# Optimization experiments

Measured on AMD Instinct MI355X. Metric: run time of the kernel, lower is better.

The kernel has to match this reference:

```python
import jax, jax.numpy as jnp
import numpy as np

N, E = 20000, 320000
IN_C, HID, OUT_C, HEADS = 512, 32, 40, 8
NEG_SLOPE = 0.2


def setup_inputs() -> dict:
    key = jax.random.key(0)
    ks = jax.random.split(key, 10)
    x = jax.random.normal(ks[0], (N, IN_C), dtype=jnp.float32)
    edge_index = jax.random.randint(ks[1], (2, E), 0, N, dtype=jnp.int64)
    s1 = 1.0 / np.sqrt(IN_C)
    s2 = 1.0 / np.sqrt(HEADS * HID)
    return {
        "x": x,
        "edge_index": edge_index,
        "w1": jax.random.normal(ks[2], (IN_C, HEADS * HID), dtype=jnp.float32) * s1,
        "att_src1": jax.random.normal(ks[3], (HEADS, HID), dtype=jnp.float32) * s2,
        "att_dst1": jax.random.normal(ks[4], (HEADS, HID), dtype=jnp.float32) * s2,
        "b1": jnp.zeros((HEADS * HID,), dtype=jnp.float32),
        "w2": jax.random.normal(ks[5], (HEADS * HID, OUT_C), dtype=jnp.float32) * s2,
        "att_src2": jax.random.normal(ks[6], (1, OUT_C), dtype=jnp.float32) * 0.15,
        "att_dst2": jax.random.normal(ks[7], (1, OUT_C), dtype=jnp.float32) * 0.15,
        "b2": jnp.zeros((OUT_C,), dtype=jnp.float32),
    }


def gat_conv(x, src, dst, w, att_src, att_dst, bias, heads, out_c, concat):
    n = x.shape[0]
    h = (x @ w).reshape(n, heads, out_c)            # [N,H,C]
    a_s = jnp.sum(h * att_src, axis=-1)             # [N,H]
    a_d = jnp.sum(h * att_dst, axis=-1)             # [N,H]
    e = jax.nn.leaky_relu(a_s[src] + a_d[dst], NEG_SLOPE)  # [E,H]
    # segment softmax over destination nodes (self-loops guarantee nonempty)
    m = jax.ops.segment_max(e, dst, num_segments=n)
    e = jnp.exp(e - m[dst])
    z = jax.ops.segment_sum(e, dst, num_segments=n)
    alpha = e / (z[dst] + 1e-16)                    # [E,H]
    msg = alpha[:, :, None] * h[src]                # [E,H,C]
    out = jax.ops.segment_sum(msg, dst, num_segments=n)  # [N,H,C]
    out = out.reshape(n, heads * out_c) if concat else out.mean(axis=1)
    return out + bias


def reference(x, edge_index, w1, att_src1, att_dst1, b1, w2, att_src2, att_dst2, b2):
    n = x.shape[0]
    loops = jnp.arange(n, dtype=edge_index.dtype)
    src = jnp.concatenate([edge_index[0], loops])
    dst = jnp.concatenate([edge_index[1], loops])
    h = gat_conv(x, src, dst, w1, att_src1, att_dst1, b1, HEADS, HID, True)
    h = jax.nn.elu(h)
    out = gat_conv(h, src, dst, w2, att_src2, att_dst2, b2, 1, OUT_C, False)
    return jax.nn.log_softmax(out, axis=1)
```

## Files before the change

### kernel.cpp

```cpp
#include <hip/hip_runtime.h>
#include <hip/hip_bf16.h>
#include <math.h>

#define N_NODES 20000
#define N_EDGES 320000
#define ET (N_EDGES + N_NODES)
#define IN_C 512
#define HEADS 8
#define HID 32
#define HH (HEADS * HID)
#define OUT_C 40
#define NEG_SLOPE 0.2f

typedef __attribute__((ext_vector_type(8))) short short8;
typedef __attribute__((ext_vector_type(4))) float floatx4;

static __device__ __forceinline__ unsigned short f2bf(float f) {
  __hip_bfloat16 h = __float2bfloat16(f);
  return *(unsigned short*)&h;
}
static __device__ __forceinline__ float bf2f_lo(unsigned int u) {
  return __uint_as_float(u << 16);
}
static __device__ __forceinline__ float bf2f_hi(unsigned int u) {
  return __uint_as_float(u & 0xFFFF0000u);
}

#define WCONV_BLOCKS (IN_C * HH / 256)
#define W2CONV_BLOCKS (HH * OUT_C / 256)
#define COUNT_BLOCKS ((ET + 255) / 256)
__global__ __launch_bounds__(256) void prep_kernel(
    const float* __restrict__ w1, const float* __restrict__ w2,
    const int* __restrict__ ei, unsigned short* __restrict__ wbT,
    unsigned short* __restrict__ w2bT, int* __restrict__ deg) {
  if (blockIdx.x < WCONV_BLOCKS) {
    int j = blockIdx.x * 256 + threadIdx.x;
    int k = j >> 8, n = j & 255;
    wbT[(size_t)n * IN_C + k] = f2bf(w1[j]);
  } else if (blockIdx.x < WCONV_BLOCKS + W2CONV_BLOCKS) {
    int j = (blockIdx.x - WCONV_BLOCKS) * 256 + threadIdx.x;
    int k = j / OUT_C, oc = j % OUT_C;
    w2bT[oc * HH + k] = f2bf(w2[j]);
  } else {
    int e = (blockIdx.x - WCONV_BLOCKS - W2CONV_BLOCKS) * 256 + threadIdx.x;
    if (e < ET) {
      int dst = (e < N_EDGES) ? ei[N_EDGES + e] : (e - N_EDGES);
      atomicAdd(&deg[dst], 1);
    }
  }
}

#define BM 64
#define BN 128
#define BK 32
#define APAD 40
#define GY ((N_NODES + BM - 1) / BM)
#define GEMM_BLOCKS (2 * GY)
__global__ __launch_bounds__(256) void gemm1_kernel(
    const float* __restrict__ X, const unsigned short* __restrict__ BT,
    const float* __restrict__ bias, unsigned short* __restrict__ C,
    const int* __restrict__ deg, int* __restrict__ offs, int* __restrict__ cursor) {
  if (blockIdx.x >= GEMM_BLOCKS) {
    __shared__ int wsum[4];
    int t = threadIdx.x;
    int4 buf[20];
    int s = 0;
    if (t < 250) {
      const int4* dp = (const int4*)deg + t * 20;
#pragma unroll
      for (int i = 0; i < 20; i++) {
        buf[i] = dp[i];
        s += buf[i].x + buf[i].y + buf[i].z + buf[i].w;
      }
    }
    int lane = t & 63, w = t >> 6;
    int inc = s;
    for (int o = 1; o < 64; o <<= 1) {
      int u = __shfl_up(inc, o, 64);
      if (lane >= o) inc += u;
    }
    if (lane == 63) wsum[w] = inc;
    __syncthreads();
    int waveOff = 0;
    for (int i = 0; i < w; i++) waveOff += wsum[i];
    int running = waveOff + inc - s;
    if (t < 250) {
      int base = t * 80;
#pragma unroll
      for (int i = 0; i < 20; i++) {
        int4 v = buf[i];
        int4 o;
        o.x = running;
        o.y = o.x + v.x;
        o.z = o.y + v.y;
        o.w = o.z + v.z;
        running = o.w + v.w;
        *(int4*)(offs + base + i * 4) = o;
        *(int4*)(cursor + base + i * 4) = o;
      }
    }
    if (t == 0) offs[N_NODES] = ET;
    return;
  }
  __shared__ unsigned short As[BM][APAD];
  __shared__ unsigned short Bs[BN][APAD];
  const int tid = threadIdx.x;
  const int lane = tid & 63, wave = tid >> 6;
  const int wm = (wave & 1) * 32;
  const int wn = (wave >> 1) * 64;
  const int r16 = lane & 15, q = lane >> 4;
  const int bx = blockIdx.x & 1, by = blockIdx.x >> 1;
  const int rowBase = by * BM;
  const int colBase = bx * BN;
  floatx4 acc[2][4] = {};

  for (int k0 = 0; k0 < IN_C; k0 += BK) {
    {
      int row = tid >> 2, kc = (tid & 3) * 8;
      int arow = rowBase + row;
      float4 v0 = make_float4(0.f, 0.f, 0.f, 0.f), v1 = v0;
      if (arow < N_NODES) {
        const float* p = X + (size_t)arow * IN_C + k0 + kc;
        v0 = *(const float4*)p;
        v1 = *(const float4*)(p + 4);
      }
      unsigned short tmp[8] = {f2bf(v0.x), f2bf(v0.y), f2bf(v0.z), f2bf(v0.w),
                               f2bf(v1.x), f2bf(v1.y), f2bf(v1.z), f2bf(v1.w)};
      *(float4*)&As[row][kc] = *(const float4*)tmp;
    }
#pragma unroll
    for (int i = 0; i < 2; i++) {
      int c = tid + i * 256;
      int row = c >> 2, kc = (c & 3) * 8;
      float4 v = *(const float4*)(BT + (size_t)(colBase + row) * IN_C + k0 + kc);
      *(float4*)&Bs[row][kc] = v;
    }
    __syncthreads();
    short8 afrag[2], bfrag[4];
#pragma unroll
    for (int mt = 0; mt < 2; mt++)
      afrag[mt] = *(const short8*)&As[wm + mt * 16 + r16][q * 8];
#pragma unroll
    for (int nt = 0; nt < 4; nt++)
      bfrag[nt] = *(const short8*)&Bs[wn + nt * 16 + r16][q * 8];
#pragma unroll
    for (int mt = 0; mt < 2; mt++)
#pragma unroll
      for (int nt = 0; nt < 4; nt++)
        acc[mt][nt] = __builtin_amdgcn_mfma_f32_16x16x32_bf16(
            afrag[mt], bfrag[nt], acc[mt][nt], 0, 0, 0);
    __syncthreads();
  }
#pragma unroll
  for (int mt = 0; mt < 2; mt++) {
#pragma unroll
    for (int nt = 0; nt < 4; nt++) {
      int col = colBase + wn + nt * 16 + r16;
      float bb = bias[col];
#pragma unroll
      for (int r = 0; r < 4; r++) {
        int row = rowBase + wm + mt * 16 + q * 4 + r;
        if (row < N_NODES) C[(size_t)row * HH + col] = f2bf(acc[mt][nt][r] + bb);
      }
    }
  }
}

#define FILL_BLOCKS ((ET + 255) / 256)
#define ATTN1_BLOCKS (N_NODES / 4)
__global__ __launch_bounds__(256) void fill_attn1_kernel(
    const int* __restrict__ ei, int* __restrict__ cursor, int* __restrict__ csr,
    const unsigned short* __restrict__ h1b, const float* __restrict__ asrc,
    const float* __restrict__ adst, float* __restrict__ as1, float* __restrict__ ad1) {
  if (blockIdx.x < FILL_BLOCKS) {
    int e = blockIdx.x * 256 + threadIdx.x;
    if (e >= ET) return;
    int src, dst;
    if (e < N_EDGES) { src = ei[e]; dst = ei[N_EDGES + e]; }
    else { src = e - N_EDGES; dst = src; }
    int pos = atomicAdd(&cursor[dst], 1);
    csr[pos] = src;
  } else {
    int wave = threadIdx.x >> 6, lane = threadIdx.x & 63;
    int n = (blockIdx.x - FILL_BLOCKS) * 4 + wave;
    int c4 = lane * 4;
    uint2 raw = *(const uint2*)(h1b + (size_t)n * HH + c4);
    float h0 = bf2f_lo(raw.x), h1 = bf2f_hi(raw.x);
    float h2 = bf2f_lo(raw.y), h3 = bf2f_hi(raw.y);
    float4 sa = *(const float4*)(asrc + c4);
    float4 sd = *(const float4*)(adst + c4);
    float ps = h0 * sa.x + h1 * sa.y + h2 * sa.z + h3 * sa.w;
    float pd = h0 * sd.x + h1 * sd.y + h2 * sd.z + h3 * sd.w;
#pragma unroll
    for (int o = 4; o > 0; o >>= 1) {
      ps += __shfl_down(ps, o, 8);
      pd += __shfl_down(pd, o, 8);
    }
    if ((lane & 7) == 0) {
      as1[n * HEADS + (lane >> 3)] = ps;
      ad1[n * HEADS + (lane >> 3)] = pd;
    }
  }
}

#define NPB 16
#define H2ROW 264
__global__ __launch_bounds__(256) void layer1_fused_kernel(
    const unsigned short* __restrict__ h1b, const float* __restrict__ as1,
    const float* __restrict__ ad1, const int* __restrict__ offs,
    const int* __restrict__ csr, const float* __restrict__ b1,
    const unsigned short* __restrict__ w2bT, const float* __restrict__ b2,
    const float* __restrict__ asrc2, const float* __restrict__ adst2,
    float* __restrict__ h3, float* __restrict__ as2, float* __restrict__ ad2) {
  __shared__ __align__(16) unsigned short h2s[NPB][H2ROW];
  __shared__ float psum[3][NPB], pdsum[3][NPB];
  const int tid = threadIdx.x;
  const int wave = tid >> 6, lane = tid & 63;
  const int r16 = lane & 15, q = lane >> 4;
  const int nodeBase = blockIdx.x * NPB;

  short8 bfrag[8];
  float sa = 0.f, sd = 0.f, b2c = 0.f;
  if (wave < 3) {
    int col = wave * 16 + r16;
    int colc = (col < OUT_C) ? col : 0;
#pragma unroll
    for (int s = 0; s < 8; s++)
      bfrag[s] = *(const short8*)(w2bT + colc * HH + s * 32 + q * 8);
    if (col < OUT_C) { sa = asrc2[col]; sd = adst2[col]; b2c = b2[col]; }
  }

  const int strm = lane >> 4;
  const int l16 = lane & 15;
  const int c16 = l16 * 16;
  const int head = l16 >> 1;
  float4 bb0 = *(const float4*)(b1 + c16);
  float4 bb1 = *(const float4*)(b1 + c16 + 4);
  float4 bb2 = *(const float4*)(b1 + c16 + 8);
  float4 bb3 = *(const float4*)(b1 + c16 + 12);
  for (int i = 0; i < 4; i++) {
    int local = wave * 4 + i;
    int n = nodeBase + local;
    int beg = offs[n], end = offs[n + 1];
    float ad = ad1[n * HEADS + head];
    float acc[16] = {};
    float l = 0.f;
#pragma unroll 2
    for (int k = beg + strm; k < end; k += 4) {
      int src = csr[k];
      float e = as1[src * HEADS + head] + ad;
      e = (e > 0.f) ? e : NEG_SLOPE * e;
      float p = __expf(e);
      l += p;
      const unsigned short* hp = h1b + ((unsigned)src << 8) + c16;
      uint4 r0 = *(const uint4*)hp;
      uint4 r1 = *(const uint4*)(hp + 8);
      acc[0]  = fmaf(p, bf2f_lo(r0.x), acc[0]);
      acc[1]  = fmaf(p, bf2f_hi(r0.x), acc[1]);
      acc[2]  = fmaf(p, bf2f_lo(r0.y), acc[2]);
      acc[3]  = fmaf(p, bf2f_hi(r0.y), acc[3]);
      acc[4]  = fmaf(p, bf2f_lo(r0.z), acc[4]);
      acc[5]  = fmaf(p, bf2f_hi(r0.z), acc[5]);
      acc[6]  = fmaf(p, bf2f_lo(r0.w), acc[6]);
      acc[7]  = fmaf(p, bf2f_hi(r0.w), acc[7]);
      acc[8]  = fmaf(p, bf2f_lo(r1.x), acc[8]);
      acc[9]  = fmaf(p, bf2f_hi(r1.x), acc[9]);
      acc[10] = fmaf(p, bf2f_lo(r1.y), acc[10]);
      acc[11] = fmaf(p, bf2f_hi(r1.y), acc[11]);
      acc[12] = fmaf(p, bf2f_lo(r1.z), acc[12]);
      acc[13] = fmaf(p, bf2f_hi(r1.z), acc[13]);
      acc[14] = fmaf(p, bf2f_lo(r1.w), acc[14]);
      acc[15] = fmaf(p, bf2f_hi(r1.w), acc[15]);
    }
#pragma unroll
    for (int j = 0; j < 16; j++) {
      acc[j] += __shfl_xor(acc[j], 16, 64);
      acc[j] += __shfl_xor(acc[j], 32, 64);
    }
    l += __shfl_xor(l, 16, 64);
    l += __shfl_xor(l, 32, 64);
    if (strm == 0) {
      float li = 1.f / (l + 1e-16f);
      float v[16];
      v[0]  = acc[0]  * li + bb0.x; v[1]  = acc[1]  * li + bb0.y;
      v[2]  = acc[2]  * li + bb0.z; v[3]  = acc[3]  * li + bb0.w;
      v[4]  = acc[4]  * li + bb1.x; v[5]  = acc[5]  * li + bb1.y;
      v[6]  = acc[6]  * li + bb1.z; v[7]  = acc[7]  * li + bb1.w;
      v[8]  = acc[8]  * li + bb2.x; v[9]  = acc[9]  * li + bb2.y;
      v[10] = acc[10] * li + bb2.z; v[11] = acc[11] * li + bb2.w;
      v[12] = acc[12] * li + bb3.x; v[13] = acc[13] * li + bb3.y;
      v[14] = acc[14] * li + bb3.z; v[15] = acc[15] * li + bb3.w;
      unsigned short o16[16];
#pragma unroll
      for (int j = 0; j < 16; j++) {
        float e = (v[j] > 0.f) ? v[j] : expm1f(v[j]);
        o16[j] = f2bf(e);
      }
      *(uint4*)&h2s[local][c16] = *(const uint4*)&o16[0];
      *(uint4*)&h2s[local][c16 + 8] = *(const uint4*)&o16[8];
    }
  }
  __syncthreads();

  if (wave < 3) {
    floatx4 dacc = {};
#pragma unroll
    for (int s = 0; s < 8; s++) {
      short8 afrag = *(const short8*)&h2s[r16][s * 32 + q * 8];
      dacc = __builtin_amdgcn_mfma_f32_16x16x32_bf16(afrag, bfrag[s], dacc, 0, 0, 0);
    }
    int col = wave * 16 + r16;
    float psr[4], pdr[4];
#pragma unroll
    for (int r = 0; r < 4; r++) {
      float val = dacc[r] + b2c;
      if (col < OUT_C)
        h3[(size_t)(nodeBase + q * 4 + r) * OUT_C + col] = val;
      psr[r] = val * sa;
      pdr[r] = val * sd;
    }
#pragma unroll
    for (int o = 8; o > 0; o >>= 1) {
#pragma unroll
      for (int r = 0; r < 4; r++) {
        psr[r] += __shfl_down(psr[r], o, 16);
        pdr[r] += __shfl_down(pdr[r], o, 16);
      }
    }
    if (r16 == 0) {
#pragma unroll
      for (int r = 0; r < 4; r++) {
        psum[wave][q * 4 + r] = psr[r];
        pdsum[wave][q * 4 + r] = pdr[r];
      }
    }
  }
  __syncthreads();
  if (tid < NPB) {
    as2[nodeBase + tid] = psum[0][tid] + psum[1][tid] + psum[2][tid];
    ad2[nodeBase + tid] = pdsum[0][tid] + pdsum[1][tid] + pdsum[2][tid];
  }
}

__global__ __launch_bounds__(256) void agg2_kernel(
    const float* __restrict__ h3, const float* __restrict__ as2,
    const float* __restrict__ ad2, const int* __restrict__ offs,
    const int* __restrict__ csr, const float* __restrict__ b2,
    float* __restrict__ out) {
  int n = blockIdx.x * 4 + (threadIdx.x >> 6);
  int t = threadIdx.x & 63;
  bool act = (t < OUT_C);
  int beg = offs[n], end = offs[n + 1];
  float ad = ad2[n];
  float l0 = 0.f, l1 = 0.f, a0 = 0.f, a1 = 0.f;
  int k = beg;
  for (; k + 1 < end; k += 2) {
    int s0 = csr[k], s1 = csr[k + 1];
    float e0 = as2[s0] + ad, e1 = as2[s1] + ad;
    e0 = (e0 > 0.f) ? e0 : NEG_SLOPE * e0;
    e1 = (e1 > 0.f) ? e1 : NEG_SLOPE * e1;
    float p0 = __expf(e0), p1 = __expf(e1);
    l0 += p0; l1 += p1;
    float h0 = act ? h3[(size_t)s0 * OUT_C + t] : 0.f;
    float h1 = act ? h3[(size_t)s1 * OUT_C + t] : 0.f;
    a0 = fmaf(p0, h0, a0);
    a1 = fmaf(p1, h1, a1);
  }
  if (k < end) {
    int s0 = csr[k];
    float e0 = as2[s0] + ad;
    e0 = (e0 > 0.f) ? e0 : NEG_SLOPE * e0;
    float p0 = __expf(e0);
    l0 += p0;
    float h0 = act ? h3[(size_t)s0 * OUT_C + t] : 0.f;
    a0 = fmaf(p0, h0, a0);
  }
  float l = l0 + l1, acc = a0 + a1;
  float v = acc / (l + 1e-16f) + (act ? b2[t] : 0.f);
  float x = act ? v : -INFINITY;
  float mx = x;
  for (int o = 32; o > 0; o >>= 1) mx = fmaxf(mx, __shfl_down(mx, o, 64));
  mx = __shfl(mx, 0, 64);
  float ex = act ? __expf(v - mx) : 0.f;
  float s = ex;
  for (int o = 32; o > 0; o >>= 1) s += __shfl_down(s, o, 64);
  s = __shfl(s, 0, 64);
  if (act) out[(size_t)n * OUT_C + t] = v - mx - logf(s);
}

extern "C" void kernel_launch(void* const* d_in, const int* in_sizes, int n_in,
                              void* d_out, int out_size, void* d_ws, size_t ws_size,
                              hipStream_t stream) {
  const float* x     = (const float*)d_in[0];
  const int*   ei    = (const int*)d_in[1];
  const float* w1    = (const float*)d_in[2];
  const float* asrc1 = (const float*)d_in[3];
  const float* adst1 = (const float*)d_in[4];
  const float* b1    = (const float*)d_in[5];
  const float* w2    = (const float*)d_in[6];
  const float* asrc2 = (const float*)d_in[7];
  const float* adst2 = (const float*)d_in[8];
  const float* b2    = (const float*)d_in[9];
  float* out = (float*)d_out;

  float* fw = (float*)d_ws;
  float* as1   = fw;  fw += (size_t)N_NODES * HEADS;
  float* ad1   = fw;  fw += (size_t)N_NODES * HEADS;
  float* h3    = fw;  fw += (size_t)N_NODES * OUT_C;
  float* as2   = fw;  fw += N_NODES;
  float* ad2   = fw;  fw += N_NODES;
  unsigned short* h1b  = (unsigned short*)fw;  fw += (size_t)N_NODES * HH / 2;
  unsigned short* wbT  = (unsigned short*)fw;  fw += (size_t)IN_C * HH / 2;
  unsigned short* w2bT = (unsigned short*)fw;  fw += (size_t)HH * OUT_C / 2;
  int* deg    = (int*)fw;
  int* offs   = deg + N_NODES;
  int* cursor = offs + N_NODES + 4;
  int* csr    = cursor + N_NODES;

  hipMemsetAsync(deg, 0, N_NODES * sizeof(int), stream);

  prep_kernel<<<WCONV_BLOCKS + W2CONV_BLOCKS + COUNT_BLOCKS, 256, 0, stream>>>(
      w1, w2, ei, wbT, w2bT, deg);
  gemm1_kernel<<<GEMM_BLOCKS + 1, 256, 0, stream>>>(x, wbT, b1, h1b, deg, offs, cursor);
  fill_attn1_kernel<<<FILL_BLOCKS + ATTN1_BLOCKS, 256, 0, stream>>>(
      ei, cursor, csr, h1b, asrc1, adst1, as1, ad1);
  layer1_fused_kernel<<<N_NODES / NPB, 256, 0, stream>>>(
      h1b, as1, ad1, offs, csr, b1, w2bT, b2, asrc2, adst2, h3, as2, ad2);
  agg2_kernel<<<N_NODES / 4, 256, 0, stream>>>(h3, as2, ad2, offs, csr, b2, out);
}
```

Measured before the change: 232.4 us.

## Store layer-1 features head-major and aggregate per head with XCC-aware scheduling

The GEMM1 output and attention scores are now stored head-major ([head][node][32]), so each head's features form a contiguous 1.28 MB slab. The fused layer-1 kernel is split into a persistent per-head aggregation kernel and a separate GEMM2/attention kernel. In the aggregation kernel, blocks pick heads starting from their XCC id and take node chunks from per-head atomic counters, so each XCC's L2 holds one head's working set. This trades an extra global round trip for the h2 intermediate and an extra launch against better cache locality in the random gathers.

```diff
diff --git a/kernel.cpp b/kernel.cpp
--- a/kernel.cpp
+++ b/kernel.cpp
@@ -24,6 +24,11 @@
 }
 static __device__ __forceinline__ float bf2f_hi(unsigned int u) {
   return __uint_as_float(u & 0xFFFF0000u);
+}
+static __device__ __forceinline__ unsigned get_xcc() {
+  unsigned x;
+  asm volatile("s_getreg_b32 %0, hwreg(HW_REG_XCC_ID)" : "=s"(x));
+  return x & 7;
 }
 
 #define WCONV_BLOCKS (IN_C * HH / 256)
@@ -156,11 +161,13 @@
 #pragma unroll
     for (int nt = 0; nt < 4; nt++) {
       int col = colBase + wn + nt * 16 + r16;
+      int head = col >> 5, ch = col & 31;
       float bb = bias[col];
 #pragma unroll
       for (int r = 0; r < 4; r++) {
         int row = rowBase + wm + mt * 16 + q * 4 + r;
-        if (row < N_NODES) C[(size_t)row * HH + col] = f2bf(acc[mt][nt][r] + bb);
+        if (row < N_NODES)
+          C[(((size_t)head * N_NODES + row) << 5) + ch] = f2bf(acc[mt][nt][r] + bb);
       }
     }
   }
@@ -170,8 +177,8 @@
 #define ATTN1_BLOCKS (N_NODES / 4)
 __global__ __launch_bounds__(256) void fill_attn1_kernel(
     const int* __restrict__ ei, int* __restrict__ cursor, int* __restrict__ csr,
-    const unsigned short* __restrict__ h1b, const float* __restrict__ asrc,
-    const float* __restrict__ adst, float* __restrict__ as1, float* __restrict__ ad1) {
+    const unsigned short* __restrict__ h1hm, const float* __restrict__ asrc,
+    const float* __restrict__ adst, float* __restrict__ as1hm, float* __restrict__ ad1hm) {
   if (blockIdx.x < FILL_BLOCKS) {
     int e = blockIdx.x * 256 + threadIdx.x;
     if (e >= ET) return;
@@ -183,12 +190,13 @@
   } else {
     int wave = threadIdx.x >> 6, lane = threadIdx.x & 63;
     int n = (blockIdx.x - FILL_BLOCKS) * 4 + wave;
-    int c4 = lane * 4;
-    uint2 raw = *(const uint2*)(h1b + (size_t)n * HH + c4);
+    int head = lane >> 3;
+    int ch = (lane & 7) * 4;
+    uint2 raw = *(const uint2*)(h1hm + (((size_t)head * N_NODES + n) << 5) + ch);
     float h0 = bf2f_lo(raw.x), h1 = bf2f_hi(raw.x);
     float h2 = bf2f_lo(raw.y), h3 = bf2f_hi(raw.y);
-    float4 sa = *(const float4*)(asrc + c4);
-    float4 sd = *(const float4*)(adst + c4);
+    float4 sa = *(const float4*)(asrc + lane * 4);
+    float4 sd = *(const float4*)(adst + lane * 4);
     float ps = h0 * sa.x + h1 * sa.y + h2 * sa.z + h3 * sa.w;
     float pd = h0 * sd.x + h1 * sd.y + h2 * sd.z + h3 * sd.w;
 #pragma unroll
@@ -197,142 +205,115 @@
       pd += __shfl_down(pd, o, 8);
     }
     if ((lane & 7) == 0) {
-      as1[n * HEADS + (lane >> 3)] = ps;
-      ad1[n * HEADS + (lane >> 3)] = pd;
+      as1hm[(size_t)head * N_NODES + n] = ps;
+      ad1hm[(size_t)head * N_NODES + n] = pd;
+    }
+  }
+}
+
+#define CHUNK 32
+#define AGG1_BLOCKS 1024
+__global__ __launch_bounds__(256) void agg1_hm_kernel(
+    const unsigned short* __restrict__ h1hm, const float* __restrict__ as1hm,
+    const float* __restrict__ ad1hm, const int* __restrict__ offs,
+    const int* __restrict__ csr, const float* __restrict__ b1,
+    unsigned short* __restrict__ h2hm, int* __restrict__ hctr) {
+  __shared__ int sh_pos;
+  const unsigned myx = get_xcc();
+  const int grp = threadIdx.x >> 3;
+  const int l8 = threadIdx.x & 7;
+  for (int hh = 0; hh < HEADS; hh++) {
+    int h = (myx + hh) & 7;
+    const float* as1h = as1hm + (size_t)h * N_NODES;
+    const float* ad1h = ad1hm + (size_t)h * N_NODES;
+    const unsigned short* h1h = h1hm + ((size_t)h * N_NODES << 5);
+    unsigned short* h2h = h2hm + ((size_t)h * N_NODES << 5);
+    float4 bb = *(const float4*)(b1 + h * 32 + l8 * 4);
+    while (true) {
+      if (threadIdx.x == 0) sh_pos = atomicAdd(&hctr[h], CHUNK);
+      __syncthreads();
+      int pos = sh_pos;
+      __syncthreads();
+      if (pos >= N_NODES) break;
+      int n = pos + grp;
+      int beg = offs[n], end = offs[n + 1];
+      float ad = ad1h[n];
+      float a0 = 0.f, a1 = 0.f, a2 = 0.f, a3 = 0.f, l = 0.f;
+      int src = csr[beg];
+      for (int k = beg; k < end; k++) {
+        int nsrc = (k + 1 < end) ? csr[k + 1] : 0;
+        uint2 raw = *(const uint2*)(h1h + ((size_t)src << 5) + l8 * 4);
+        float e = as1h[src] + ad;
+        e = (e > 0.f) ? e : NEG_SLOPE * e;
+        float p = __expf(e);
+        l += p;
+        a0 = fmaf(p, bf2f_lo(raw.x), a0);
+        a1 = fmaf(p, bf2f_hi(raw.x), a1);
+        a2 = fmaf(p, bf2f_lo(raw.y), a2);
+        a3 = fmaf(p, bf2f_hi(raw.y), a3);
+        src = nsrc;
+      }
+      float li = 1.f / (l + 1e-16f);
+      float v0 = a0 * li + bb.x, v1 = a1 * li + bb.y;
+      float v2 = a2 * li + bb.z, v3 = a3 * li + bb.w;
+      v0 = (v0 > 0.f) ? v0 : expm1f(v0);
+      v1 = (v1 > 0.f) ? v1 : expm1f(v1);
+      v2 = (v2 > 0.f) ? v2 : expm1f(v2);
+      v3 = (v3 > 0.f) ? v3 : expm1f(v3);
+      unsigned short o4[4] = {f2bf(v0), f2bf(v1), f2bf(v2), f2bf(v3)};
+      *(uint2*)(h2h + ((size_t)n << 5) + l8 * 4) = *(const uint2*)o4;
     }
   }
 }
 
 #define NPB 16
-#define H2ROW 264
-__global__ __launch_bounds__(256) void layer1_fused_kernel(
-    const unsigned short* __restrict__ h1b, const float* __restrict__ as1,
-    const float* __restrict__ ad1, const int* __restrict__ offs,
-    const int* __restrict__ csr, const float* __restrict__ b1,
-    const unsigned short* __restrict__ w2bT, const float* __restrict__ b2,
-    const float* __restrict__ asrc2, const float* __restrict__ adst2,
-    float* __restrict__ h3, float* __restrict__ as2, float* __restrict__ ad2) {
-  __shared__ __align__(16) unsigned short h2s[NPB][H2ROW];
+__global__ __launch_bounds__(192) void gemm2_attn2_kernel(
+    const unsigned short* __restrict__ h2hm, const unsigned short* __restrict__ w2bT,
+    const float* __restrict__ b2, const float* __restrict__ asrc2,
+    const float* __restrict__ adst2, float* __restrict__ h3,
+    float* __restrict__ as2, float* __restrict__ ad2) {
   __shared__ float psum[3][NPB], pdsum[3][NPB];
   const int tid = threadIdx.x;
   const int wave = tid >> 6, lane = tid & 63;
   const int r16 = lane & 15, q = lane >> 4;
   const int nodeBase = blockIdx.x * NPB;
-
+  int col = wave * 16 + r16;
+  int colc = (col < OUT_C) ? col : 0;
+  float sa = 0.f, sd = 0.f, b2c = 0.f;
+  if (col < OUT_C) { sa = asrc2[col]; sd = adst2[col]; b2c = b2[col]; }
   short8 bfrag[8];
-  float sa = 0.f, sd = 0.f, b2c = 0.f;
-  if (wave < 3) {
-    int col = wave * 16 + r16;
-    int colc = (col < OUT_C) ? col : 0;
-#pragma unroll
-    for (int s = 0; s < 8; s++)
-      bfrag[s] = *(const short8*)(w2bT + colc * HH + s * 32 + q * 8);
-    if (col < OUT_C) { sa = asrc2[col]; sd = adst2[col]; b2c = b2[col]; }
-  }
-
-  const int strm = lane >> 4;
-  const int l16 = lane & 15;
-  const int c16 = l16 * 16;
-  const int head = l16 >> 1;
-  float4 bb0 = *(const float4*)(b1 + c16);
-  float4 bb1 = *(const float4*)(b1 + c16 + 4);
-  float4 bb2 = *(const float4*)(b1 + c16 + 8);
-  float4 bb3 = *(const float4*)(b1 + c16 + 12);
-  for (int i = 0; i < 4; i++) {
-    int local = wave * 4 + i;
-    int n = nodeBase + local;
-    int beg = offs[n], end = offs[n + 1];
-    float ad = ad1[n * HEADS + head];
-    float acc[16] = {};
-    float l = 0.f;
-#pragma unroll 2
-    for (int k = beg + strm; k < end; k += 4) {
-      int src = csr[k];
-      float e = as1[src * HEADS + head] + ad;
-      e = (e > 0.f) ? e : NEG_SLOPE * e;
-      float p = __expf(e);
-      l += p;
-      const unsigned short* hp = h1b + ((unsigned)src << 8) + c16;
-      uint4 r0 = *(const uint4*)hp;
-      uint4 r1 = *(const uint4*)(hp + 8);
-      acc[0]  = fmaf(p, bf2f_lo(r0.x), acc[0]);
-      acc[1]  = fmaf(p, bf2f_hi(r0.x), acc[1]);
-      acc[2]  = fmaf(p, bf2f_lo(r0.y), acc[2]);
-      acc[3]  = fmaf(p, bf2f_hi(r0.y), acc[3]);
-      acc[4]  = fmaf(p, bf2f_lo(r0.z), acc[4]);
-      acc[5]  = fmaf(p, bf2f_hi(r0.z), acc[5]);
-      acc[6]  = fmaf(p, bf2f_lo(r0.w), acc[6]);
-      acc[7]  = fmaf(p, bf2f_hi(r0.w), acc[7]);
-      acc[8]  = fmaf(p, bf2f_lo(r1.x), acc[8]);
-      acc[9]  = fmaf(p, bf2f_hi(r1.x), acc[9]);
-      acc[10] = fmaf(p, bf2f_lo(r1.y), acc[10]);
-      acc[11] = fmaf(p, bf2f_hi(r1.y), acc[11]);
-      acc[12] = fmaf(p, bf2f_lo(r1.z), acc[12]);
-      acc[13] = fmaf(p, bf2f_hi(r1.z), acc[13]);
-      acc[14] = fmaf(p, bf2f_lo(r1.w), acc[14]);
-      acc[15] = fmaf(p, bf2f_hi(r1.w), acc[15]);
-    }
-#pragma unroll
-    for (int j = 0; j < 16; j++) {
-      acc[j] += __shfl_xor(acc[j], 16, 64);
-      acc[j] += __shfl_xor(acc[j], 32, 64);
-    }
-    l += __shfl_xor(l, 16, 64);
-    l += __shfl_xor(l, 32, 64);
-    if (strm == 0) {
-      float li = 1.f / (l + 1e-16f);
-      float v[16];
-      v[0]  = acc[0]  * li + bb0.x; v[1]  = acc[1]  * li + bb0.y;
-      v[2]  = acc[2]  * li + bb0.z; v[3]  = acc[3]  * li + bb0.w;
-      v[4]  = acc[4]  * li + bb1.x; v[5]  = acc[5]  * li + bb1.y;
-      v[6]  = acc[6]  * li + bb1.z; v[7]  = acc[7]  * li + bb1.w;
-      v[8]  = acc[8]  * li + bb2.x; v[9]  = acc[9]  * li + bb2.y;
-      v[10] = acc[10] * li + bb2.z; v[11] = acc[11] * li + bb2.w;
-      v[12] = acc[12] * li + bb3.x; v[13] = acc[13] * li + bb3.y;
-      v[14] = acc[14] * li + bb3.z; v[15] = acc[15] * li + bb3.w;
-      unsigned short o16[16];
-#pragma unroll
-      for (int j = 0; j < 16; j++) {
-        float e = (v[j] > 0.f) ? v[j] : expm1f(v[j]);
-        o16[j] = f2bf(e);
-      }
-      *(uint4*)&h2s[local][c16] = *(const uint4*)&o16[0];
-      *(uint4*)&h2s[local][c16 + 8] = *(const uint4*)&o16[8];
-    }
-  }
-  __syncthreads();
-
-  if (wave < 3) {
-    floatx4 dacc = {};
-#pragma unroll
-    for (int s = 0; s < 8; s++) {
-      short8 afrag = *(const short8*)&h2s[r16][s * 32 + q * 8];
-      dacc = __builtin_amdgcn_mfma_f32_16x16x32_bf16(afrag, bfrag[s], dacc, 0, 0, 0);
-    }
-    int col = wave * 16 + r16;
-    float psr[4], pdr[4];
+#pragma unroll
+  for (int s = 0; s < 8; s++)
+    bfrag[s] = *(const short8*)(w2bT + colc * HH + s * 32 + q * 8);
+  floatx4 dacc = {};
+#pragma unroll
+  for (int s = 0; s < 8; s++) {
+    short8 afrag = *(const short8*)(
+        h2hm + (((size_t)s * N_NODES + nodeBase + r16) << 5) + q * 8);
+    dacc = __builtin_amdgcn_mfma_f32_16x16x32_bf16(afrag, bfrag[s], dacc, 0, 0, 0);
+  }
+  float psr[4], pdr[4];
+#pragma unroll
+  for (int r = 0; r < 4; r++) {
+    float val = dacc[r] + b2c;
+    if (col < OUT_C)
+      h3[(size_t)(nodeBase + q * 4 + r) * OUT_C + col] = val;
+    psr[r] = val * sa;
+    pdr[r] = val * sd;
+  }
+#pragma unroll
+  for (int o = 8; o > 0; o >>= 1) {
 #pragma unroll
     for (int r = 0; r < 4; r++) {
-      float val = dacc[r] + b2c;
-      if (col < OUT_C)
-        h3[(size_t)(nodeBase + q * 4 + r) * OUT_C + col] = val;
-      psr[r] = val * sa;
-      pdr[r] = val * sd;
-    }
-#pragma unroll
-    for (int o = 8; o > 0; o >>= 1) {
-#pragma unroll
-      for (int r = 0; r < 4; r++) {
-        psr[r] += __shfl_down(psr[r], o, 16);
-        pdr[r] += __shfl_down(pdr[r], o, 16);
-      }
-    }
-    if (r16 == 0) {
-#pragma unroll
-      for (int r = 0; r < 4; r++) {
-        psum[wave][q * 4 + r] = psr[r];
-        pdsum[wave][q * 4 + r] = pdr[r];
-      }
+      psr[r] += __shfl_down(psr[r], o, 16);
+      pdr[r] += __shfl_down(pdr[r], o, 16);
+    }
+  }
+  if (r16 == 0) {
+#pragma unroll
+    for (int r = 0; r < 4; r++) {
+      psum[wave][q * 4 + r] = psr[r];
+      pdsum[wave][q * 4 + r] = pdr[r];
     }
   }
   __syncthreads();
@@ -404,27 +385,31 @@
   float* out = (float*)d_out;
 
   float* fw = (float*)d_ws;
-  float* as1   = fw;  fw += (size_t)N_NODES * HEADS;
-  float* ad1   = fw;  fw += (size_t)N_NODES * HEADS;
+  float* as1hm = fw;  fw += (size_t)N_NODES * HEADS;
+  float* ad1hm = fw;  fw += (size_t)N_NODES * HEADS;
   float* h3    = fw;  fw += (size_t)N_NODES * OUT_C;
   float* as2   = fw;  fw += N_NODES;
   float* ad2   = fw;  fw += N_NODES;
-  unsigned short* h1b  = (unsigned short*)fw;  fw += (size_t)N_NODES * HH / 2;
+  unsigned short* h1hm = (unsigned short*)fw;  fw += (size_t)N_NODES * HH / 2;
+  unsigned short* h2hm = (unsigned short*)fw;  fw += (size_t)N_NODES * HH / 2;
   unsigned short* wbT  = (unsigned short*)fw;  fw += (size_t)IN_C * HH / 2;
   unsigned short* w2bT = (unsigned short*)fw;  fw += (size_t)HH * OUT_C / 2;
   int* deg    = (int*)fw;
-  int* offs   = deg + N_NODES;
+  int* hctr   = deg + N_NODES;
+  int* offs   = deg + N_NODES + 8;
   int* cursor = offs + N_NODES + 4;
   int* csr    = cursor + N_NODES;
 
-  hipMemsetAsync(deg, 0, N_NODES * sizeof(int), stream);
+  hipMemsetAsync(deg, 0, (N_NODES + 8) * sizeof(int), stream);
 
   prep_kernel<<<WCONV_BLOCKS + W2CONV_BLOCKS + COUNT_BLOCKS, 256, 0, stream>>>(
       w1, w2, ei, wbT, w2bT, deg);
-  gemm1_kernel<<<GEMM_BLOCKS + 1, 256, 0, stream>>>(x, wbT, b1, h1b, deg, offs, cursor);
+  gemm1_kernel<<<GEMM_BLOCKS + 1, 256, 0, stream>>>(x, wbT, b1, h1hm, deg, offs, cursor);
   fill_attn1_kernel<<<FILL_BLOCKS + ATTN1_BLOCKS, 256, 0, stream>>>(
-      ei, cursor, csr, h1b, asrc1, adst1, as1, ad1);
-  layer1_fused_kernel<<<N_NODES / NPB, 256, 0, stream>>>(
-      h1b, as1, ad1, offs, csr, b1, w2bT, b2, asrc2, adst2, h3, as2, ad2);
+      ei, cursor, csr, h1hm, asrc1, adst1, as1hm, ad1hm);
+  agg1_hm_kernel<<<AGG1_BLOCKS, 256, 0, stream>>>(
+      h1hm, as1hm, ad1hm, offs, csr, b1, h2hm, hctr);
+  gemm2_attn2_kernel<<<N_NODES / NPB, 192, 0, stream>>>(
+      h2hm, w2bT, b2, asrc2, adst2, h3, as2, ad2);
   agg2_kernel<<<N_NODES / 4, 256, 0, stream>>>(h3, as2, ad2, offs, csr, b2, out);
 }
```

Measured after the change: 349.1 us. +50.2%, slower.

## Balance layer-1 aggregation with edge-split merge-path work and shared-memory atomics

Applied to the files above, without the earlier changes.

The layer-1 fused kernel now handles 32 destination nodes per block and splits the block's full CSR edge range evenly across 16 thread groups, instead of giving each wave four fixed nodes. Each group binary-searches its starting node and accumulates partial sums in registers with a one-edge software prefetch. It flushes those sums into a shared-memory fp32 accumulator with atomics at node boundaries. This targets load imbalance from degree variation, at the cost of a large LDS footprint, LDS atomics and an extra normalize/ELU pass before the MFMA projection, which now reloads W2 fragments per job.

```diff
diff --git a/kernel.cpp b/kernel.cpp
--- a/kernel.cpp
+++ b/kernel.cpp
@@ -203,7 +203,8 @@
   }
 }
 
-#define NPB 16
+#define NPB1 32
+#define AROW 260
 #define H2ROW 264
 __global__ __launch_bounds__(256) void layer1_fused_kernel(
     const unsigned short* __restrict__ h1b, const float* __restrict__ as1,
@@ -212,133 +213,169 @@
     const unsigned short* __restrict__ w2bT, const float* __restrict__ b2,
     const float* __restrict__ asrc2, const float* __restrict__ adst2,
     float* __restrict__ h3, float* __restrict__ as2, float* __restrict__ ad2) {
-  __shared__ __align__(16) unsigned short h2s[NPB][H2ROW];
-  __shared__ float psum[3][NPB], pdsum[3][NPB];
+  __shared__ __align__(16) float h2acc[NPB1][AROW];
+  __shared__ float lsum8[NPB1][HEADS];
+  __shared__ int soffs[NPB1 + 1];
+  __shared__ float adc[NPB1 * HEADS];
+  __shared__ float psum[3][NPB1], pdsum[3][NPB1];
   const int tid = threadIdx.x;
-  const int wave = tid >> 6, lane = tid & 63;
-  const int r16 = lane & 15, q = lane >> 4;
-  const int nodeBase = blockIdx.x * NPB;
-
-  short8 bfrag[8];
-  float sa = 0.f, sd = 0.f, b2c = 0.f;
-  if (wave < 3) {
-    int col = wave * 16 + r16;
-    int colc = (col < OUT_C) ? col : 0;
-#pragma unroll
-    for (int s = 0; s < 8; s++)
-      bfrag[s] = *(const short8*)(w2bT + colc * HH + s * 32 + q * 8);
-    if (col < OUT_C) { sa = asrc2[col]; sd = adst2[col]; b2c = b2[col]; }
-  }
-
-  const int strm = lane >> 4;
-  const int l16 = lane & 15;
-  const int c16 = l16 * 16;
-  const int head = l16 >> 1;
-  float4 bb0 = *(const float4*)(b1 + c16);
-  float4 bb1 = *(const float4*)(b1 + c16 + 4);
-  float4 bb2 = *(const float4*)(b1 + c16 + 8);
-  float4 bb3 = *(const float4*)(b1 + c16 + 12);
-  for (int i = 0; i < 4; i++) {
-    int local = wave * 4 + i;
-    int n = nodeBase + local;
-    int beg = offs[n], end = offs[n + 1];
-    float ad = ad1[n * HEADS + head];
-    float acc[16] = {};
-    float l = 0.f;
-#pragma unroll 2
-    for (int k = beg + strm; k < end; k += 4) {
-      int src = csr[k];
-      float e = as1[src * HEADS + head] + ad;
-      e = (e > 0.f) ? e : NEG_SLOPE * e;
-      float p = __expf(e);
-      l += p;
-      const unsigned short* hp = h1b + ((unsigned)src << 8) + c16;
+  const int d0 = blockIdx.x * NPB1;
+
+  for (int i = tid; i < NPB1 * AROW; i += 256) ((float*)h2acc)[i] = 0.f;
+  ((float*)lsum8)[tid] = 0.f;
+  if (tid <= NPB1) soffs[tid] = offs[d0 + tid];
+  adc[tid] = ad1[d0 * HEADS + tid];
+  __syncthreads();
+
+  {
+    const int grp = tid >> 4;
+    const int sub = tid & 15;
+    const int head = sub >> 1;
+    const int ch16 = sub * 16;
+    const int e0 = soffs[0], e1 = soffs[NPB1];
+    const int chunk = (e1 - e0 + 15) >> 4;
+    int myBeg = e0 + grp * chunk;
+    int myEnd = myBeg + chunk;
+    if (myEnd > e1) myEnd = e1;
+    if (myBeg < myEnd) {
+      int lo = 0, hi = NPB1;
+      while (hi - lo > 1) {
+        int mid = (lo + hi) >> 1;
+        if (soffs[mid] <= myBeg) lo = mid; else hi = mid;
+      }
+      int bound = soffs[lo + 1];
+      float acc[16] = {};
+      float lacc = 0.f;
+      int src = csr[myBeg];
+      const unsigned short* hp = h1b + ((unsigned)src << 8) + ch16;
       uint4 r0 = *(const uint4*)hp;
       uint4 r1 = *(const uint4*)(hp + 8);
-      acc[0]  = fmaf(p, bf2f_lo(r0.x), acc[0]);
-      acc[1]  = fmaf(p, bf2f_hi(r0.x), acc[1]);
-      acc[2]  = fmaf(p, bf2f_lo(r0.y), acc[2]);
-      acc[3]  = fmaf(p, bf2f_hi(r0.y), acc[3]);
-      acc[4]  = fmaf(p, bf2f_lo(r0.z), acc[4]);
-      acc[5]  = fmaf(p, bf2f_hi(r0.z), acc[5]);
-      acc[6]  = fmaf(p, bf2f_lo(r0.w), acc[6]);
-      acc[7]  = fmaf(p, bf2f_hi(r0.w), acc[7]);
-      acc[8]  = fmaf(p, bf2f_lo(r1.x), acc[8]);
-      acc[9]  = fmaf(p, bf2f_hi(r1.x), acc[9]);
-      acc[10] = fmaf(p, bf2f_lo(r1.y), acc[10]);
-      acc[11] = fmaf(p, bf2f_hi(r1.y), acc[11]);
-      acc[12] = fmaf(p, bf2f_lo(r1.z), acc[12]);
-      acc[13] = fmaf(p, bf2f_hi(r1.z), acc[13]);
-      acc[14] = fmaf(p, bf2f_lo(r1.w), acc[14]);
-      acc[15] = fmaf(p, bf2f_hi(r1.w), acc[15]);
-    }
-#pragma unroll
-    for (int j = 0; j < 16; j++) {
-      acc[j] += __shfl_xor(acc[j], 16, 64);
-      acc[j] += __shfl_xor(acc[j], 32, 64);
-    }
-    l += __shfl_xor(l, 16, 64);
-    l += __shfl_xor(l, 32, 64);
-    if (strm == 0) {
-      float li = 1.f / (l + 1e-16f);
-      float v[16];
-      v[0]  = acc[0]  * li + bb0.x; v[1]  = acc[1]  * li + bb0.y;
-      v[2]  = acc[2]  * li + bb0.z; v[3]  = acc[3]  * li + bb0.w;
-      v[4]  = acc[4]  * li + bb1.x; v[5]  = acc[5]  * li + bb1.y;
-      v[6]  = acc[6]  * li + bb1.z; v[7]  = acc[7]  * li + bb1.w;
-      v[8]  = acc[8]  * li + bb2.x; v[9]  = acc[9]  * li + bb2.y;
-      v[10] = acc[10] * li + bb2.z; v[11] = acc[11] * li + bb2.w;
-      v[12] = acc[12] * li + bb3.x; v[13] = acc[13] * li + bb3.y;
-      v[14] = acc[14] * li + bb3.z; v[15] = acc[15] * li + bb3.w;
-      unsigned short o16[16];
-#pragma unroll
-      for (int j = 0; j < 16; j++) {
-        float e = (v[j] > 0.f) ? v[j] : expm1f(v[j]);
-        o16[j] = f2bf(e);
-      }
-      *(uint4*)&h2s[local][c16] = *(const uint4*)&o16[0];
-      *(uint4*)&h2s[local][c16 + 8] = *(const uint4*)&o16[8];
+      float as = as1[src * HEADS + head];
+      for (int e = myBeg; e < myEnd; e++) {
+        int en = e + 1;
+        uint4 n0, n1;
+        float nas = 0.f;
+        if (en < myEnd) {
+          int nsrc = csr[en];
+          const unsigned short* np = h1b + ((unsigned)nsrc << 8) + ch16;
+          n0 = *(const uint4*)np;
+          n1 = *(const uint4*)(np + 8);
+          nas = as1[nsrc * HEADS + head];
+        } else {
+          n0 = make_uint4(0, 0, 0, 0);
+          n1 = make_uint4(0, 0, 0, 0);
+        }
+        if (e >= bound) {
+          float* arow = &h2acc[lo][ch16];
+#pragma unroll
+          for (int j = 0; j < 16; j++) atomicAdd(&arow[j], acc[j]);
+          if ((sub & 1) == 0) atomicAdd(&lsum8[lo][head], lacc);
+#pragma unroll
+          for (int j = 0; j < 16; j++) acc[j] = 0.f;
+          lacc = 0.f;
+          lo++;
+          while (soffs[lo + 1] <= e) lo++;
+          bound = soffs[lo + 1];
+        }
+        float x = as + adc[lo * HEADS + head];
+        x = (x > 0.f) ? x : NEG_SLOPE * x;
+        float p = __expf(x);
+        lacc += p;
+        acc[0]  = fmaf(p, bf2f_lo(r0.x), acc[0]);
+        acc[1]  = fmaf(p, bf2f_hi(r0.x), acc[1]);
+        acc[2]  = fmaf(p, bf2f_lo(r0.y), acc[2]);
+        acc[3]  = fmaf(p, bf2f_hi(r0.y), acc[3]);
+        acc[4]  = fmaf(p, bf2f_lo(r0.z), acc[4]);
+        acc[5]  = fmaf(p, bf2f_hi(r0.z), acc[5]);
+        acc[6]  = fmaf(p, bf2f_lo(r0.w), acc[6]);
+        acc[7]  = fmaf(p, bf2f_hi(r0.w), acc[7]);
+        acc[8]  = fmaf(p, bf2f_lo(r1.x), acc[8]);
+        acc[9]  = fmaf(p, bf2f_hi(r1.x), acc[9]);
+        acc[10] = fmaf(p, bf2f_lo(r1.y), acc[10]);
+        acc[11] = fmaf(p, bf2f_hi(r1.y), acc[11]);
+        acc[12] = fmaf(p, bf2f_lo(r1.z), acc[12]);
+        acc[13] = fmaf(p, bf2f_hi(r1.z), acc[13]);
+        acc[14] = fmaf(p, bf2f_lo(r1.w), acc[14]);
+        acc[15] = fmaf(p, bf2f_hi(r1.w), acc[15]);
+        r0 = n0; r1 = n1; as = nas;
+      }
+      float* arow = &h2acc[lo][ch16];
+#pragma unroll
+      for (int j = 0; j < 16; j++) atomicAdd(&arow[j], acc[j]);
+      if ((sub & 1) == 0) atomicAdd(&lsum8[lo][head], lacc);
     }
   }
   __syncthreads();
 
-  if (wave < 3) {
-    floatx4 dacc = {};
-#pragma unroll
-    for (int s = 0; s < 8; s++) {
-      short8 afrag = *(const short8*)&h2s[r16][s * 32 + q * 8];
-      dacc = __builtin_amdgcn_mfma_f32_16x16x32_bf16(afrag, bfrag[s], dacc, 0, 0, 0);
-    }
-    int col = wave * 16 + r16;
-    float psr[4], pdr[4];
-#pragma unroll
-    for (int r = 0; r < 4; r++) {
-      float val = dacc[r] + b2c;
-      if (col < OUT_C)
-        h3[(size_t)(nodeBase + q * 4 + r) * OUT_C + col] = val;
-      psr[r] = val * sa;
-      pdr[r] = val * sd;
-    }
-#pragma unroll
-    for (int o = 8; o > 0; o >>= 1) {
+  {
+    const int row = tid >> 3;
+    const int g = tid & 7;
+    float vals[32];
+#pragma unroll
+    for (int j = 0; j < 32; j++) vals[j] = h2acc[row][g * 32 + j];
+    float li = 1.f / (lsum8[row][g] + 1e-16f);
+    unsigned short o32[32];
+#pragma unroll
+    for (int j = 0; j < 32; j++) {
+      float v = vals[j] * li + b1[g * 32 + j];
+      v = (v > 0.f) ? v : expm1f(v);
+      o32[j] = f2bf(v);
+    }
+    __syncthreads();
+    unsigned short* h2s = (unsigned short*)h2acc;
+#pragma unroll
+    for (int j = 0; j < 4; j++)
+      *(uint4*)&h2s[row * H2ROW + g * 32 + j * 8] = *(const uint4*)&o32[j * 8];
+  }
+  __syncthreads();
+
+  {
+    const int wave = tid >> 6, lane = tid & 63;
+    const int r16 = lane & 15, q = lane >> 4;
+    const unsigned short* h2s = (const unsigned short*)h2acc;
+    for (int job = wave; job < 6; job += 4) {
+      int rt = job / 3, ct = job % 3;
+      int col = ct * 16 + r16;
+      int colc = (col < OUT_C) ? col : 0;
+      float sa = 0.f, sd = 0.f, b2c = 0.f;
+      if (col < OUT_C) { sa = asrc2[col]; sd = adst2[col]; b2c = b2[col]; }
+      floatx4 dacc = {};
+#pragma unroll
+      for (int s = 0; s < 8; s++) {
+        short8 bfrag = *(const short8*)(w2bT + colc * HH + s * 32 + q * 8);
+        short8 afrag = *(const short8*)&h2s[(rt * 16 + r16) * H2ROW + s * 32 + q * 8];
+        dacc = __builtin_amdgcn_mfma_f32_16x16x32_bf16(afrag, bfrag, dacc, 0, 0, 0);
+      }
+      float psr[4], pdr[4];
 #pragma unroll
       for (int r = 0; r < 4; r++) {
-        psr[r] += __shfl_down(psr[r], o, 16);
-        pdr[r] += __shfl_down(pdr[r], o, 16);
-      }
-    }
-    if (r16 == 0) {
-#pragma unroll
-      for (int r = 0; r < 4; r++) {
-        psum[wave][q * 4 + r] = psr[r];
-        pdsum[wave][q * 4 + r] = pdr[r];
+        float val = dacc[r] + b2c;
+        if (col < OUT_C)
+          h3[(size_t)(d0 + rt * 16 + q * 4 + r) * OUT_C + col] = val;
+        psr[r] = val * sa;
+        pdr[r] = val * sd;
+      }
+#pragma unroll
+      for (int o = 8; o > 0; o >>= 1) {
+#pragma unroll
+        for (int r = 0; r < 4; r++) {
+          psr[r] += __shfl_down(psr[r], o, 16);
+          pdr[r] += __shfl_down(pdr[r], o, 16);
+        }
+      }
+      if (r16 == 0) {
+#pragma unroll
+        for (int r = 0; r < 4; r++) {
+          psum[ct][rt * 16 + q * 4 + r] = psr[r];
+          pdsum[ct][rt * 16 + q * 4 + r] = pdr[r];
+        }
       }
     }
   }
   __syncthreads();
-  if (tid < NPB) {
-    as2[nodeBase + tid] = psum[0][tid] + psum[1][tid] + psum[2][tid];
-    ad2[nodeBase + tid] = pdsum[0][tid] + pdsum[1][tid] + pdsum[2][tid];
+  if (tid < NPB1) {
+    as2[d0 + tid] = psum[0][tid] + psum[1][tid] + psum[2][tid];
+    ad2[d0 + tid] = pdsum[0][tid] + pdsum[1][tid] + pdsum[2][tid];
   }
 }
 
@@ -424,7 +461,7 @@
   gemm1_kernel<<<GEMM_BLOCKS + 1, 256, 0, stream>>>(x, wbT, b1, h1b, deg, offs, cursor);
   fill_attn1_kernel<<<FILL_BLOCKS + ATTN1_BLOCKS, 256, 0, stream>>>(
       ei, cursor, csr, h1b, asrc1, adst1, as1, ad1);
-  layer1_fused_kernel<<<N_NODES / NPB, 256, 0, stream>>>(
+  layer1_fused_kernel<<<N_NODES / NPB1, 256, 0, stream>>>(
       h1b, as1, ad1, offs, csr, b1, w2bT, b2, asrc2, adst2, h3, as2, ad2);
   agg2_kernel<<<N_NODES / 4, 256, 0, stream>>>(h3, as2, ad2, offs, csr, b2, out);
 }
```

After: 251.5 us. 8.2% more time.
